# Kernel tuning notes

Measured on AMD Instinct MI355X. Metric: run time of the kernel, lower is better.

## Reference

```python
import jax, jax.numpy as jnp
import numpy as np
from jax import lax

INP_MODES = (4, 8, 8, 4)
OUT_MODES = (4, 8, 8, 4)
RANKS = (1, 8, 8, 8, 1)  # mat_ranks
WINDOW = (3, 3)


def setup_inputs() -> dict:
    key = jax.random.key(0)
    ks = jax.random.split(key, 7)
    d = {}
    d["x"] = jax.random.normal(ks[0], (16, 32, 32, 1024), jnp.float32)
    # conv filter: [kh, kw, 1, r0]
    d["filters"] = jax.random.normal(ks[1], (WINDOW[0], WINDOW[1], 1, RANKS[0]), jnp.float32) * (1.0 / 3.0)
    # TT cores: core_i has shape [m_i * r_{i+1}, r_i * n_i]
    for i in range(4):
        shp = (OUT_MODES[i] * RANKS[i + 1], RANKS[i] * INP_MODES[i])
        d[f"core{i}"] = jax.random.normal(ks[2 + i], shp, jnp.float32) * (1.0 / np.sqrt(shp[1]).astype(np.float32))
    d["bias"] = jnp.zeros((int(np.prod(OUT_MODES)),), jnp.float32)
    return d


def tt_conv(x, filters, cores, bias):
    B, H, W, C = x.shape  # C == prod(INP_MODES)
    r0 = filters.shape[3]
    # depthwise-style: every channel of every batch item becomes its own 1-channel map
    tmp = x.transpose(0, 3, 1, 2).reshape(B * C, H, W, 1)
    tmp = lax.conv_general_dilated(tmp, filters, window_strides=(1, 1), padding="SAME",
                                   dimension_numbers=("NHWC", "HWIO", "NHWC"))
    h, w = tmp.shape[1], tmp.shape[2]
    # [B, C, h, w, r0] -> [r0, C, B, h, w]
    tmp = tmp.reshape(B, C, h, w, r0).transpose(4, 1, 0, 2, 3)
    # chained TT-core contractions (fixed small loop over num_dim)
    for i in range(len(cores)):
        tmp = tmp.reshape(RANKS[i] * INP_MODES[i], -1)
        tmp = cores[i] @ tmp                      # [m_i * r_{i+1}, rest]
        tmp = tmp.reshape(OUT_MODES[i], -1).T     # move m_i to the back
    M = int(np.prod(OUT_MODES))
    out = tmp.reshape(-1, h, w, M) + bias
    return jax.nn.relu(out)


def reference(x, filters, core0, core1, core2, core3, bias):
    return tt_conv(x, filters, [core0, core1, core2, core3], bias)
```

## Files before the change

kernel.cpp:

```cpp
#include <hip/hip_runtime.h>
#include <hip/hip_bf16.h>
#include <stdint.h>

typedef __attribute__((ext_vector_type(8))) short short8;
typedef __attribute__((ext_vector_type(4))) float f32x4;

__device__ inline unsigned short f2bf(float f) {
  union { float f; unsigned u; } v; v.f = f;
  unsigned r = v.u + 0x7fffu + ((v.u >> 16) & 1u);
  return (unsigned short)(r >> 16);
}
__device__ inline float bf2f(unsigned short u) {
  union { unsigned u; float f; } v; v.u = ((unsigned)u) << 16; return v.f;
}

__global__ __launch_bounds__(256) void tt_prep(
    const float* __restrict__ x, const float* __restrict__ filt,
    const float* __restrict__ c0, const float* __restrict__ c1,
    const float* __restrict__ c2, const float* __restrict__ c3,
    unsigned short* __restrict__ Tb, unsigned short* __restrict__ D) {
  __shared__ __align__(16) char smem[40960];
  const int tid = threadIdx.x;
  const int bid = blockIdx.x;

  if (bid < 256) {
    unsigned short* Lb = (unsigned short*)smem;
    unsigned short* Rb = (unsigned short*)(smem + 16384);
    for (int i = tid; i < 8192; i += 256) {
      int n1 = i & 7, n0 = (i >> 3) & 3, r2 = (i >> 5) & 7, m1 = (i >> 8) & 7, m0 = i >> 11;
      float s = 0.f;
#pragma unroll
      for (int r1 = 0; r1 < 8; ++r1)
        s += c0[(m0 * 8 + r1) * 4 + n0] * c1[(m1 * 8 + r2) * 64 + r1 * 8 + n1];
      Lb[i] = f2bf(s);
    }
    for (int i = tid; i < 8192; i += 256) {
      int n3 = i & 3, n2 = (i >> 2) & 7, m3 = (i >> 5) & 3, m2 = (i >> 7) & 7, r2 = i >> 10;
      float s = 0.f;
#pragma unroll
      for (int r3 = 0; r3 < 8; ++r3)
        s += c2[(m2 * 8 + r3) * 64 + r2 * 8 + n2] * c3[m3 * 32 + r3 * 4 + n3];
      Rb[i] = f2bf(s);
    }
    __syncthreads();
    int base = bid * 4096;
    for (int j = 0; j < 16; ++j) {
      int g = base + j * 256 + tid;
      int m = g >> 10, n = g & 1023;
      int m0 = m >> 8, m1 = (m >> 5) & 7, m2 = (m >> 2) & 7, m3 = m & 3;
      int n0 = n >> 8, n1 = (n >> 5) & 7, n2 = (n >> 2) & 7, n3 = n & 3;
      float s = 0.f;
#pragma unroll
      for (int r2 = 0; r2 < 8; ++r2)
        s += bf2f(Lb[(((m0 * 8 + m1) * 8 + r2) * 4 + n0) * 8 + n1]) *
             bf2f(Rb[(((r2 * 8 + m2) * 4 + m3) * 8 + n2) * 4 + n3]);
      Tb[(size_t)m * 1024 + n] = f2bf(s);
    }
    return;
  }

  float (*xs)[32][32] = (float(*)[32][32])smem;
  int cb = bid - 256;
  int cg = cb & 31, strip = (cb >> 5) & 3, b = cb >> 7;
  int h0 = strip * 8;
  float4 z4; z4.x = z4.y = z4.z = z4.w = 0.f;
#pragma unroll
  for (int i = 0; i < 10; ++i) {
    int j = tid + 256 * i;
    int row = j >> 8, w = (j >> 3) & 31, c4 = j & 7;
    int gh = h0 - 1 + row;
    float4 v = z4;
    if ((unsigned)gh < 32u)
      v = *reinterpret_cast<const float4*>(x + ((size_t)((b * 32 + gh) * 32 + w)) * 1024 + cg * 32 + c4 * 4);
    *reinterpret_cast<float4*>(&xs[row][w][c4 * 4]) = v;
  }
  float F[9];
#pragma unroll
  for (int i = 0; i < 9; ++i) F[i] = filt[i];
  __syncthreads();

  int c4 = tid & 7, w = tid >> 3;
#define LD3(r, d0, d1, d2) { \
    d1 = *reinterpret_cast<const float4*>(&xs[r][w][c4 * 4]); \
    d0 = (w > 0)  ? *reinterpret_cast<const float4*>(&xs[r][w - 1][c4 * 4]) : z4; \
    d2 = (w < 31) ? *reinterpret_cast<const float4*>(&xs[r][w + 1][c4 * 4]) : z4; }
#define ACC4(a, f, v) { a.x += (f) * v.x; a.y += (f) * v.y; a.z += (f) * v.z; a.w += (f) * v.w; }
  float4 a00, a01, a02, a10, a11, a12, a20, a21, a22;
  LD3(0, a00, a01, a02);
  LD3(1, a10, a11, a12);
#pragma unroll
  for (int h = 0; h < 8; ++h) {
    LD3(h + 2, a20, a21, a22);
    float4 s = z4;
    ACC4(s, F[0], a00); ACC4(s, F[1], a01); ACC4(s, F[2], a02);
    ACC4(s, F[3], a10); ACC4(s, F[4], a11); ACC4(s, F[5], a12);
    ACC4(s, F[6], a20); ACC4(s, F[7], a21); ACC4(s, F[8], a22);
    ushort4 o;
    o.x = f2bf(s.x); o.y = f2bf(s.y); o.z = f2bf(s.z); o.w = f2bf(s.w);
    *reinterpret_cast<ushort4*>(&D[((size_t)(b * 1024 + (h0 + h) * 32 + w)) * 1024 + cg * 32 + c4 * 4]) = o;
    a00 = a10; a01 = a11; a02 = a12;
    a10 = a20; a11 = a21; a12 = a22;
  }
#undef LD3
#undef ACC4
}

__device__ inline void stage16(const unsigned short* g, unsigned short* l) {
  __builtin_amdgcn_global_load_lds(
      (const __attribute__((address_space(1))) void*)g,
      (__attribute__((address_space(3))) void*)l, 16, 0, 0);
}

__global__ __launch_bounds__(512, 2) void tt_gemm_rb(
    const unsigned short* __restrict__ A,
    const unsigned short* __restrict__ Bt,
    const float* __restrict__ bias,
    float* __restrict__ C) {
  __shared__ unsigned short lds[4][16384];
  const int tid = threadIdx.x;
  const int lane = tid & 63, wave = tid >> 6;
  const int wr = wave >> 2, wc = wave & 3;
  const int lr = lane & 15, kc = lane >> 4;

  int lin = blockIdx.x + blockIdx.y * 64;
  int Lg = ((lin & 7) << 5) | (lin >> 3);
  int brow = (Lg & 63) * 256;
  int bcol = (Lg >> 6) * 256;

  int row0, k0, row1, k1;
  { int q = tid;       int li = q >> 3, c = (q & 7) ^ (li & 7); row0 = 2 * li + (c >> 2); k0 = (c & 3) * 8; }
  { int q = tid + 512; int li = q >> 3, c = (q & 7) ^ (li & 7); row1 = 2 * li + (c >> 2); k1 = (c & 3) * 8; }
  const unsigned short* pa0 = A + (size_t)(brow + row0) * 1024 + k0;
  const unsigned short* pa1 = A + (size_t)(brow + row1) * 1024 + k1;
  const unsigned short* pb0 = Bt + (size_t)(bcol + row0) * 1024 + k0;
  const unsigned short* pb1 = Bt + (size_t)(bcol + row1) * 1024 + k1;
  const int la0 = tid * 8, la1 = (tid + 512) * 8;

  int offA[8], offB[4];
#pragma unroll
  for (int m = 0; m < 8; ++m) {
    int row = wr * 128 + m * 16 + lr;
    int li = row >> 1, sl = (row & 1) * 4 + kc;
    offA[m] = (li * 8 + (sl ^ (li & 7))) * 8;
  }
#pragma unroll
  for (int n = 0; n < 4; ++n) {
    int row = wc * 64 + n * 16 + lr;
    int li = row >> 1, sl = (row & 1) * 4 + kc;
    offB[n] = 8192 + (li * 8 + (sl ^ (li & 7))) * 8;
  }

  f32x4 acc[8][4] = {};
  short8 a0[8], b0[4], a1[8], b1[4];

#define STAGE(S, T) { \
    stage16(pa0 + (T) * 32, &lds[S][la0]); \
    stage16(pa1 + (T) * 32, &lds[S][la1]); \
    stage16(pb0 + (T) * 32, &lds[S][8192 + la0]); \
    stage16(pb1 + (T) * 32, &lds[S][8192 + la1]); }

#define READF(AF, BF, S) { \
    _Pragma("unroll") for (int m = 0; m < 8; ++m) \
      AF[m] = *reinterpret_cast<const short8*>(&lds[S][offA[m]]); \
    _Pragma("unroll") for (int n = 0; n < 4; ++n) \
      BF[n] = *reinterpret_cast<const short8*>(&lds[S][offB[n]]); }

#define MFMAS(AF, BF) { \
    _Pragma("unroll") for (int m = 0; m < 8; ++m) \
      _Pragma("unroll") for (int n = 0; n < 4; ++n) \
        acc[m][n] = __builtin_amdgcn_mfma_f32_16x16x32_bf16(BF[n], AF[m], acc[m][n], 0, 0, 0); }

#define ITER(T, AFc, BFc, AFn, BFn, DOSTAGE, VMS) { \
    asm volatile("s_waitcnt lgkmcnt(12)" ::: "memory"); \
    asm volatile("s_waitcnt vmcnt(" VMS ")" ::: "memory"); \
    __builtin_amdgcn_s_barrier(); \
    if (DOSTAGE) STAGE(((T) + 3) & 3, (T) + 3); \
    READF(AFn, BFn, ((T) + 1) & 3); \
    MFMAS(AFc, BFc); }

  STAGE(0, 0); STAGE(1, 1); STAGE(2, 2);
  asm volatile("s_waitcnt vmcnt(8)" ::: "memory");
  __builtin_amdgcn_s_barrier();
  READF(a0, b0, 0);

  for (int tp = 0; tp < 14; ++tp) {
    int t = 2 * tp;
    ITER(t,     a0, b0, a1, b1, 1, "4")
    ITER(t + 1, a1, b1, a0, b0, 1, "4")
  }
  ITER(28, a0, b0, a1, b1, 1, "4")
  ITER(29, a1, b1, a0, b0, 0, "4")
  ITER(30, a0, b0, a1, b1, 0, "0")
  MFMAS(a1, b1);

#undef ITER
#undef MFMAS
#undef READF
#undef STAGE

#pragma unroll
  for (int n = 0; n < 4; ++n) {
    int col = bcol + wc * 64 + n * 16 + kc * 4;
    float4 bv = *reinterpret_cast<const float4*>(&bias[col]);
#pragma unroll
    for (int m = 0; m < 8; ++m) {
      int row = brow + wr * 128 + m * 16 + lr;
      f32x4 v = acc[m][n];
      float4 o;
      o.x = v[0] + bv.x; o.y = v[1] + bv.y; o.z = v[2] + bv.z; o.w = v[3] + bv.w;
      o.x = o.x > 0.f ? o.x : 0.f;
      o.y = o.y > 0.f ? o.y : 0.f;
      o.z = o.z > 0.f ? o.z : 0.f;
      o.w = o.w > 0.f ? o.w : 0.f;
      *reinterpret_cast<float4*>(&C[(size_t)row * 1024 + col]) = o;
    }
  }
}

extern "C" void kernel_launch(void* const* d_in, const int* in_sizes, int n_in,
                              void* d_out, int out_size, void* d_ws, size_t ws_size,
                              hipStream_t stream) {
  const float* x = (const float*)d_in[0];
  const float* filt = (const float*)d_in[1];
  const float* c0 = (const float*)d_in[2];
  const float* c1 = (const float*)d_in[3];
  const float* c2 = (const float*)d_in[4];
  const float* c3 = (const float*)d_in[5];
  const float* bias = (const float*)d_in[6];
  float* out = (float*)d_out;

  unsigned short* Tb = (unsigned short*)d_ws;
  unsigned short* D = Tb + (size_t)1024 * 1024;

  tt_prep<<<2304, 256, 0, stream>>>(x, filt, c0, c1, c2, c3, Tb, D);
  dim3 grid(64, 4);
  tt_gemm_rb<<<grid, 512, 0, stream>>>(D, Tb, bias, out);
}
```

Baseline: 72.32 us.

## Write operands in MFMA fragment layout and drop LDS staging in GEMM

The prep kernel now stores the conv output and the fused TT matrix directly in a pre-swizzled per-lane fragment order. This lets the GEMM load each MFMA operand with one contiguous 16-byte global load per lane, so the LDS staging, barriers and waitcnt pipeline can be removed. Each wave now loads its own fragments straight from global memory with register double buffering. The trade-off is that data shared between waves is no longer reused through LDS, which raises global/L2 traffic and exposes load latency to the MFMA loop.

```diff
diff --git a/kernel.cpp b/kernel.cpp
--- a/kernel.cpp
+++ b/kernel.cpp
@@ -14,11 +14,12 @@
   union { unsigned u; float f; } v; v.u = ((unsigned)u) << 16; return v.f;
 }
 
+
 __global__ __launch_bounds__(256) void tt_prep(
     const float* __restrict__ x, const float* __restrict__ filt,
     const float* __restrict__ c0, const float* __restrict__ c1,
     const float* __restrict__ c2, const float* __restrict__ c3,
-    unsigned short* __restrict__ Tb, unsigned short* __restrict__ D) {
+    unsigned short* __restrict__ Tp, unsigned short* __restrict__ Dp) {
   __shared__ __align__(16) char smem[40960];
   const int tid = threadIdx.x;
   const int bid = blockIdx.x;
@@ -54,7 +55,9 @@
       for (int r2 = 0; r2 < 8; ++r2)
         s += bf2f(Lb[(((m0 * 8 + m1) * 8 + r2) * 4 + n0) * 8 + n1]) *
              bf2f(Rb[(((r2 * 8 + m2) * 4 + m3) * 8 + n2) * 4 + n3]);
-      Tb[(size_t)m * 1024 + n] = f2bf(s);
+      int ct = m >> 6, nf = (m & 63) >> 4, lane = ((n >> 3) & 3) * 16 + (m & 15);
+      int kt = n >> 5, e = n & 7;
+      Tp[(size_t)(ct * 32 + kt) * 2048 + nf * 512 + lane * 8 + e] = f2bf(s);
     }
     return;
   }
@@ -80,6 +83,7 @@
   __syncthreads();
 
   int c4 = tid & 7, w = tid >> 3;
+  const int kchunk = (c4 >> 1) & 3, e0 = (c4 & 1) * 4;
 #define LD3(r, d0, d1, d2) { \
     d1 = *reinterpret_cast<const float4*>(&xs[r][w][c4 * 4]); \
     d0 = (w > 0)  ? *reinterpret_cast<const float4*>(&xs[r][w - 1][c4 * 4]) : z4; \
@@ -97,7 +101,10 @@
     ACC4(s, F[6], a20); ACC4(s, F[7], a21); ACC4(s, F[8], a22);
     ushort4 o;
     o.x = f2bf(s.x); o.y = f2bf(s.y); o.z = f2bf(s.z); o.w = f2bf(s.w);
-    *reinterpret_cast<ushort4*>(&D[((size_t)(b * 1024 + (h0 + h) * 32 + w)) * 1024 + cg * 32 + c4 * 4]) = o;
+    int p = b * 1024 + (h0 + h) * 32 + w;
+    int at = p >> 7, m = (p & 127) >> 4, lane = kchunk * 16 + (p & 15);
+    *reinterpret_cast<ushort4*>(
+        &Dp[(size_t)(at * 32 + cg) * 8192 + m * 512 + lane * 8 + e0]) = o;
     a00 = a10; a01 = a11; a02 = a12;
     a10 = a20; a11 = a21; a12 = a22;
   }
@@ -105,18 +112,11 @@
 #undef ACC4
 }
 
-__device__ inline void stage16(const unsigned short* g, unsigned short* l) {
-  __builtin_amdgcn_global_load_lds(
-      (const __attribute__((address_space(1))) void*)g,
-      (__attribute__((address_space(3))) void*)l, 16, 0, 0);
-}
-
-__global__ __launch_bounds__(512, 2) void tt_gemm_rb(
-    const unsigned short* __restrict__ A,
-    const unsigned short* __restrict__ Bt,
+__global__ __launch_bounds__(512, 2) void tt_gemm_nl(
+    const unsigned short* __restrict__ Dp,
+    const unsigned short* __restrict__ Tp,
     const float* __restrict__ bias,
     float* __restrict__ C) {
-  __shared__ unsigned short lds[4][16384];
   const int tid = threadIdx.x;
   const int lane = tid & 63, wave = tid >> 6;
   const int wr = wave >> 2, wc = wave & 3;
@@ -124,80 +124,45 @@
 
   int lin = blockIdx.x + blockIdx.y * 64;
   int Lg = ((lin & 7) << 5) | (lin >> 3);
-  int brow = (Lg & 63) * 256;
-  int bcol = (Lg >> 6) * 256;
-
-  int row0, k0, row1, k1;
-  { int q = tid;       int li = q >> 3, c = (q & 7) ^ (li & 7); row0 = 2 * li + (c >> 2); k0 = (c & 3) * 8; }
-  { int q = tid + 512; int li = q >> 3, c = (q & 7) ^ (li & 7); row1 = 2 * li + (c >> 2); k1 = (c & 3) * 8; }
-  const unsigned short* pa0 = A + (size_t)(brow + row0) * 1024 + k0;
-  const unsigned short* pa1 = A + (size_t)(brow + row1) * 1024 + k1;
-  const unsigned short* pb0 = Bt + (size_t)(bcol + row0) * 1024 + k0;
-  const unsigned short* pb1 = Bt + (size_t)(bcol + row1) * 1024 + k1;
-  const int la0 = tid * 8, la1 = (tid + 512) * 8;
-
-  int offA[8], offB[4];
-#pragma unroll
-  for (int m = 0; m < 8; ++m) {
-    int row = wr * 128 + m * 16 + lr;
-    int li = row >> 1, sl = (row & 1) * 4 + kc;
-    offA[m] = (li * 8 + (sl ^ (li & 7))) * 8;
-  }
-#pragma unroll
-  for (int n = 0; n < 4; ++n) {
-    int row = wc * 64 + n * 16 + lr;
-    int li = row >> 1, sl = (row & 1) * 4 + kc;
-    offB[n] = 8192 + (li * 8 + (sl ^ (li & 7))) * 8;
-  }
+  int bR = Lg & 63;
+  int bC = Lg >> 6;
+  int at = bR * 2 + wr;
+  int ct = bC * 4 + wc;
+
+  const unsigned short* aB = Dp + (size_t)at * 32 * 8192 + lane * 8;
+  const unsigned short* bB = Tp + (size_t)ct * 32 * 2048 + lane * 8;
 
   f32x4 acc[8][4] = {};
   short8 a0[8], b0[4], a1[8], b1[4];
 
-#define STAGE(S, T) { \
-    stage16(pa0 + (T) * 32, &lds[S][la0]); \
-    stage16(pa1 + (T) * 32, &lds[S][la1]); \
-    stage16(pb0 + (T) * 32, &lds[S][8192 + la0]); \
-    stage16(pb1 + (T) * 32, &lds[S][8192 + la1]); }
-
-#define READF(AF, BF, S) { \
+#define LD(AF, BF, KT) { \
+    const unsigned short* ap = aB + (size_t)(KT) * 8192; \
+    const unsigned short* bp = bB + (size_t)(KT) * 2048; \
     _Pragma("unroll") for (int m = 0; m < 8; ++m) \
-      AF[m] = *reinterpret_cast<const short8*>(&lds[S][offA[m]]); \
+      AF[m] = *reinterpret_cast<const short8*>(ap + m * 512); \
     _Pragma("unroll") for (int n = 0; n < 4; ++n) \
-      BF[n] = *reinterpret_cast<const short8*>(&lds[S][offB[n]]); }
-
-#define MFMAS(AF, BF) { \
+      BF[n] = *reinterpret_cast<const short8*>(bp + n * 512); }
+
+#define FM(AF, BF) { \
     _Pragma("unroll") for (int m = 0; m < 8; ++m) \
       _Pragma("unroll") for (int n = 0; n < 4; ++n) \
         acc[m][n] = __builtin_amdgcn_mfma_f32_16x16x32_bf16(BF[n], AF[m], acc[m][n], 0, 0, 0); }
 
-#define ITER(T, AFc, BFc, AFn, BFn, DOSTAGE, VMS) { \
-    asm volatile("s_waitcnt lgkmcnt(12)" ::: "memory"); \
-    asm volatile("s_waitcnt vmcnt(" VMS ")" ::: "memory"); \
-    __builtin_amdgcn_s_barrier(); \
-    if (DOSTAGE) STAGE(((T) + 3) & 3, (T) + 3); \
-    READF(AFn, BFn, ((T) + 1) & 3); \
-    MFMAS(AFc, BFc); }
-
-  STAGE(0, 0); STAGE(1, 1); STAGE(2, 2);
-  asm volatile("s_waitcnt vmcnt(8)" ::: "memory");
-  __builtin_amdgcn_s_barrier();
-  READF(a0, b0, 0);
-
-  for (int tp = 0; tp < 14; ++tp) {
-    int t = 2 * tp;
-    ITER(t,     a0, b0, a1, b1, 1, "4")
-    ITER(t + 1, a1, b1, a0, b0, 1, "4")
-  }
-  ITER(28, a0, b0, a1, b1, 1, "4")
-  ITER(29, a1, b1, a0, b0, 0, "4")
-  ITER(30, a0, b0, a1, b1, 0, "0")
-  MFMAS(a1, b1);
-
-#undef ITER
-#undef MFMAS
-#undef READF
-#undef STAGE
-
+  LD(a0, b0, 0);
+  for (int kt = 0; kt < 30; kt += 2) {
+    LD(a1, b1, kt + 1);
+    FM(a0, b0);
+    LD(a0, b0, kt + 2);
+    FM(a1, b1);
+  }
+  LD(a1, b1, 31);
+  FM(a0, b0);
+  FM(a1, b1);
+
+#undef LD
+#undef FM
+
+  int brow = bR * 256, bcol = bC * 256;
 #pragma unroll
   for (int n = 0; n < 4; ++n) {
     int col = bcol + wc * 64 + n * 16 + kc * 4;
@@ -229,10 +194,10 @@
   const float* bias = (const float*)d_in[6];
   float* out = (float*)d_out;
 
-  unsigned short* Tb = (unsigned short*)d_ws;
-  unsigned short* D = Tb + (size_t)1024 * 1024;
-
-  tt_prep<<<2304, 256, 0, stream>>>(x, filt, c0, c1, c2, c3, Tb, D);
+  unsigned short* Tp = (unsigned short*)d_ws;
+  unsigned short* Dp = Tp + (size_t)1024 * 1024;
+
+  tt_prep<<<2304, 256, 0, stream>>>(x, filt, c0, c1, c2, c3, Tp, Dp);
   dim3 grid(64, 4);
-  tt_gemm_rb<<<grid, 512, 0, stream>>>(D, Tb, bias, out);
-}
+  tt_gemm_nl<<<grid, 512, 0, stream>>>(Dp, Tp, bias, out);
+}
```

Measured after the change: 82.25 us. 1.14x slower.
